# Kernel optimization log

Hardware: AMD Instinct MI355X
Metric: run time of the kernel (lower is better)

Reference implementation:

```python
import jax, jax.numpy as jnp
import numpy as np

B, S, E, H, L, D, G, V = 32, 256, 300, 256, 4000, 256, 512, 50000
LIN1, LIN2 = 512, 256  # linear_size


def _glorot(key, shape):
    fan_in, fan_out = shape[-1], shape[-2] if len(shape) > 1 else shape[-1]
    std = np.sqrt(2.0 / (fan_in + fan_out))
    return jax.random.normal(key, shape, dtype=jnp.float32) * std


def setup_inputs() -> dict:
    key = jax.random.key(0)
    ks = jax.random.split(key, 20)
    tokens = jax.random.randint(ks[0], (B, S), 1, V)  # avoid padding_idx=0
    emb_table = jax.random.normal(ks[1], (V, E), dtype=jnp.float32) * 0.1
    emb_table = emb_table.at[0].set(0.0)  # padding row
    # bidirectional LSTM (1 layer), torch gate order i,f,g,o
    w_ih_f = _glorot(ks[2], (4 * H, E));  w_hh_f = _glorot(ks[3], (4 * H, H))
    b_f = jnp.zeros((4 * H,), jnp.float32)
    w_ih_b = _glorot(ks[4], (4 * H, E));  w_hh_b = _glorot(ks[5], (4 * H, H))
    b_b = jnp.zeros((4 * H,), jnp.float32)
    # MLAttention: Linear(2H -> L, bias=False)
    attn_w = _glorot(ks[6], (L, 2 * H))
    # label graph branch
    label_emb = _glorot(ks[7], (L, D))
    adj_raw = (jax.random.uniform(ks[8], (L, L)) < 0.004).astype(jnp.float32)
    adj_raw = adj_raw + jnp.eye(L, dtype=jnp.float32)
    deg = jnp.sum(adj_raw, axis=1, keepdims=True)
    adj = adj_raw / deg  # row-normalized dense adjacency [L, L]
    gcn_w = _glorot(ks[9], (D, G));  gcn_b = jnp.zeros((G,), jnp.float32)
    # MLLinear([2H+G, 512, 256], 1)
    w1 = _glorot(ks[10], (2 * H + G, LIN1));  b1 = jnp.zeros((LIN1,), jnp.float32)
    w2 = _glorot(ks[11], (LIN1, LIN2));       b2 = jnp.zeros((LIN2,), jnp.float32)
    w_out = _glorot(ks[12], (LIN2, 1));       b_out = jnp.zeros((1,), jnp.float32)
    return dict(tokens=tokens, emb_table=emb_table,
                w_ih_f=w_ih_f, w_hh_f=w_hh_f, b_f=b_f,
                w_ih_b=w_ih_b, w_hh_b=w_hh_b, b_b=b_b,
                attn_w=attn_w, label_emb=label_emb, adj=adj,
                gcn_w=gcn_w, gcn_b=gcn_b,
                w1=w1, b1=b1, w2=w2, b2=b2, w_out=w_out, b_out=b_out)


def _lstm_dir(x_gates, w_hh, reverse):
    # x_gates: [B, S, 4H] precomputed input projections (+bias)
    def step(carry, xt):
        h, c = carry
        gates = xt + h @ w_hh.T
        i, f, g, o = jnp.split(gates, 4, axis=-1)
        c = jax.nn.sigmoid(f) * c + jax.nn.sigmoid(i) * jnp.tanh(g)
        h = jax.nn.sigmoid(o) * jnp.tanh(c)
        return (h, c), h
    b = x_gates.shape[0]
    init = (jnp.zeros((b, H), x_gates.dtype), jnp.zeros((b, H), x_gates.dtype))
    _, hs = jax.lax.scan(step, init, jnp.swapaxes(x_gates, 0, 1), reverse=reverse)
    return jnp.swapaxes(hs, 0, 1)  # [B, S, H]


def reference(tokens, emb_table, w_ih_f, w_hh_f, b_f, w_ih_b, w_hh_b, b_b,
              attn_w, label_emb, adj, gcn_w, gcn_b,
              w1, b1, w2, b2, w_out, b_out):
    masks = tokens != 0  # [B, S]
    emb_out = emb_table[tokens]  # [B, S, E]
    # bidirectional LSTM -> [B, S, 2H]
    gates_f = jnp.einsum('bse,ge->bsg', emb_out, w_ih_f) + b_f
    gates_b = jnp.einsum('bse,ge->bsg', emb_out, w_ih_b) + b_b
    rnn_out = jnp.concatenate([_lstm_dir(gates_f, w_hh_f, False),
                               _lstm_dir(gates_b, w_hh_b, True)], axis=-1)
    # MLAttention: per-label attention over sequence
    scores = jnp.einsum('bsh,lh->bls', rnn_out, attn_w)  # [B, L, S]
    scores = jnp.where(masks[:, None, :], scores, jnp.float32(-1e9))
    attn = jax.nn.softmax(scores, axis=-1)
    attn_out = jnp.einsum('bls,bsh->blh', attn, rnn_out)  # [B, L, 2H]
    # GCN over label graph: relu(A @ (X W) + b), single layer [D -> G]
    gcn_out = jax.nn.relu(adj @ (label_emb @ gcn_w) + gcn_b)  # [L, G]
    gcn_out = jnp.broadcast_to(gcn_out[None], (attn_out.shape[0], L, G))
    # concat fusion + MLLinear([2H+G, 512, 256], 1)
    x = jnp.concatenate([attn_out, gcn_out], axis=-1)  # [B, L, 2H+G]
    x = jax.nn.relu(x @ w1 + b1)
    x = jax.nn.relu(x @ w2 + b2)
    out = jnp.squeeze(x @ w_out + b_out, -1)  # [B, L]
    return out
```

## Files before the change

### kernel.cpp

```cpp
#include <hip/hip_runtime.h>
#include <hip/hip_bf16.h>
#include <math.h>


typedef __attribute__((ext_vector_type(8))) short bfrag;
typedef __attribute__((ext_vector_type(4))) float ffrag;

__device__ __forceinline__ ushort f2bf(float x) {
    union { float f; unsigned u; } c; c.f = x;
    const unsigned r = c.u + 0x7fffu + ((c.u >> 16) & 1u);
    return (ushort)(r >> 16);
}
__device__ __forceinline__ float bf2f(ushort h) {
    union { unsigned u; float f; } c; c.u = (unsigned)h << 16;
    return c.f;
}

template<bool BIAS, bool ADDROW, bool RELU, bool OUTF, bool OUTS>
__global__ __launch_bounds__(256) void mgemm_k(
    const ushort* __restrict__ A, const ushort* __restrict__ B,
    float* __restrict__ Cf, ushort* __restrict__ Cs,
    int M, int N, int K, int lda, int ldb, int ldc, int ldcs,
    long abs_, long bbs_, long cbs_, long csbs_,
    const float* __restrict__ bias,
    const float* __restrict__ addrow, int addmod, int ldadd)
{
    const int tid = threadIdx.x;
    const int ln = tid & 63;
    const int wv = tid >> 6;
    const int wm = wv >> 1, wn = wv & 1;
    const int m0 = blockIdx.x * 128, n0 = blockIdx.y * 128;
    const int z = blockIdx.z;
    A += (size_t)z * abs_;
    B += (size_t)z * bbs_;

    __shared__ ushort Ah[128 * 40], Al[128 * 40], Bh[128 * 40], Bl[128 * 40];

    ffrag acc[4][4];
#pragma unroll
    for (int i = 0; i < 4; ++i)
#pragma unroll
        for (int j = 0; j < 4; ++j) acc[i][j] = ffrag{0.f, 0.f, 0.f, 0.f};

    const int sr = tid >> 1;
    const int sk = (tid & 1) * 16;
    const int am = min(m0 + sr, M - 1);
    const int bn = n0 + sr;
    const int fr = ln & 15;
    const int fk = (ln >> 4) * 8;

    const ushort* arow = A + (size_t)am * lda + sk;
    const ushort* brow = B + (size_t)bn * ldb + sk;

    bfrag ah0, ah1, al0, al1, bh0, bh1, bl0, bl1;
    {
        const ushort* ap = arow;
        const ushort* bp = brow;
        ah0 = *(const bfrag*)ap;       ah1 = *(const bfrag*)(ap + 8);
        al0 = *(const bfrag*)(ap + K); al1 = *(const bfrag*)(ap + K + 8);
        bh0 = *(const bfrag*)bp;       bh1 = *(const bfrag*)(bp + 8);
        bl0 = *(const bfrag*)(bp + K); bl1 = *(const bfrag*)(bp + K + 8);
    }

    for (int k0 = 0; k0 < K; k0 += 32) {
        __syncthreads();
        *(bfrag*)&Ah[sr * 40 + sk] = ah0;  *(bfrag*)&Ah[sr * 40 + sk + 8] = ah1;
        *(bfrag*)&Al[sr * 40 + sk] = al0;  *(bfrag*)&Al[sr * 40 + sk + 8] = al1;
        *(bfrag*)&Bh[sr * 40 + sk] = bh0;  *(bfrag*)&Bh[sr * 40 + sk + 8] = bh1;
        *(bfrag*)&Bl[sr * 40 + sk] = bl0;  *(bfrag*)&Bl[sr * 40 + sk + 8] = bl1;
        __syncthreads();
        if (k0 + 32 < K) {
            const ushort* ap = arow + k0 + 32;
            const ushort* bp = brow + k0 + 32;
            ah0 = *(const bfrag*)ap;       ah1 = *(const bfrag*)(ap + 8);
            al0 = *(const bfrag*)(ap + K); al1 = *(const bfrag*)(ap + K + 8);
            bh0 = *(const bfrag*)bp;       bh1 = *(const bfrag*)(bp + 8);
            bl0 = *(const bfrag*)(bp + K); bl1 = *(const bfrag*)(bp + K + 8);
        }
        bfrag afh[4], afl[4];
#pragma unroll
        for (int i = 0; i < 4; ++i) {
            const int ar = (wm * 64 + i * 16 + fr) * 40 + fk;
            afh[i] = *(const bfrag*)&Ah[ar];
            afl[i] = *(const bfrag*)&Al[ar];
        }
#pragma unroll
        for (int j = 0; j < 4; ++j) {
            const int br = (wn * 64 + j * 16 + fr) * 40 + fk;
            const bfrag bfh = *(const bfrag*)&Bh[br];
            const bfrag bfl = *(const bfrag*)&Bl[br];
#pragma unroll
            for (int i = 0; i < 4; ++i) {
                acc[i][j] = __builtin_amdgcn_mfma_f32_16x16x32_bf16(afh[i], bfh, acc[i][j], 0, 0, 0);
                acc[i][j] = __builtin_amdgcn_mfma_f32_16x16x32_bf16(afh[i], bfl, acc[i][j], 0, 0, 0);
                acc[i][j] = __builtin_amdgcn_mfma_f32_16x16x32_bf16(afl[i], bfh, acc[i][j], 0, 0, 0);
            }
        }
    }

#pragma unroll
    for (int i = 0; i < 4; ++i) {
#pragma unroll
        for (int rg = 0; rg < 4; ++rg) {
            const int gm = m0 + wm * 64 + i * 16 + (ln >> 4) * 4 + rg;
            if (gm >= M) continue;
            const float* addp = ADDROW ? (addrow + (size_t)(gm % addmod) * ldadd) : nullptr;
#pragma unroll
            for (int j = 0; j < 4; ++j) {
                const int gn = n0 + wn * 64 + j * 16 + fr;
                float v = acc[i][j][rg];
                if (BIAS) v += bias[gn];
                if (ADDROW) v += addp[gn];
                if (RELU) v = fmaxf(v, 0.f);
                if (OUTF) Cf[(size_t)z * cbs_ + (size_t)gm * ldc + gn] = v;
                if (OUTS) {
                    const ushort h = f2bf(v);
                    const ushort l = f2bf(v - bf2f(h));
                    ushort* cp = Cs + (size_t)z * csbs_ + (size_t)gm * ldcs;
                    cp[gn] = h;
                    cp[N + gn] = l;
                }
            }
        }
    }
}

__global__ void gsplit_k(const float* __restrict__ src, const int* __restrict__ tok,
                         ushort* __restrict__ outp, int K, int Kpad)
{
    const int r = blockIdx.x;
    const float* s = src + (size_t)(tok ? tok[r] : r) * K;
    ushort* o = outp + (size_t)r * 2 * Kpad;
    for (int k = threadIdx.x; k < Kpad; k += blockDim.x) {
        const float x = (k < K) ? s[k] : 0.f;
        const ushort h = f2bf(x);
        const ushort l = f2bf(x - bf2f(h));
        o[k] = h;
        o[Kpad + k] = l;
    }
}

__global__ void split_k(const float* __restrict__ in, ushort* __restrict__ outp,
                        int rows, int K)
{
    const int i = blockIdx.x * 256 + threadIdx.x;
    if (i >= rows * K) return;
    const int r = i / K, k = i - r * K;
    const float x = in[i];
    const ushort h = f2bf(x);
    const ushort l = f2bf(x - bf2f(h));
    ushort* o = outp + (size_t)r * 2 * K;
    o[k] = h;
    o[K + k] = l;
}

__global__ __launch_bounds__(256) void tsplit_k(
    const float* __restrict__ in, ushort* __restrict__ outp,
    int R, int C, int ldin, long ibs, long obs)
{
    __shared__ float t[64][65];
    const int c0 = blockIdx.x * 64, r0 = blockIdx.y * 64;
    in   += (size_t)blockIdx.z * ibs;
    outp += (size_t)blockIdx.z * obs;
    const int tx = threadIdx.x & 15, ty = threadIdx.x >> 4;
#pragma unroll
    for (int i = 0; i < 4; ++i) {
        const int r = ty * 4 + i;
        const float4 v = *(const float4*)&in[(size_t)(r0 + r) * ldin + c0 + tx * 4];
        t[tx * 4 + 0][r] = v.x;
        t[tx * 4 + 1][r] = v.y;
        t[tx * 4 + 2][r] = v.z;
        t[tx * 4 + 3][r] = v.w;
    }
    __syncthreads();
    const int R2 = 2 * R;
#pragma unroll
    for (int i = 0; i < 4; ++i) {
        const int c = ty * 4 + i;
        ushort h[4], l[4];
#pragma unroll
        for (int k2 = 0; k2 < 4; ++k2) {
            const float x = t[c][tx * 4 + k2];
            h[k2] = f2bf(x);
            l[k2] = f2bf(x - bf2f(h[k2]));
        }
        uint2 hw, lw;
        hw.x = (unsigned)h[0] | ((unsigned)h[1] << 16);
        hw.y = (unsigned)h[2] | ((unsigned)h[3] << 16);
        lw.x = (unsigned)l[0] | ((unsigned)l[1] << 16);
        lw.y = (unsigned)l[2] | ((unsigned)l[3] << 16);
        *(uint2*)&outp[(size_t)(c0 + c) * R2 + r0 + tx * 4] = hw;
        *(uint2*)&outp[(size_t)(c0 + c) * R2 + R + r0 + tx * 4] = lw;
    }
}

__global__ __launch_bounds__(1024) void lstm_reg_k(
    const float* __restrict__ gxf, const float* __restrict__ gxb,
    const float* __restrict__ whf, const float* __restrict__ whb,
    float* __restrict__ rnn, float* hbuf, int* stamp)
{
    const int p = blockIdx.x;
    const int q = blockIdx.y;
    const int b = p >> 1, dir = p & 1;
    const float* xg = dir ? gxb : gxf;
    const float* W  = dir ? whb : whf;
    const int tid = threadIdx.x;
    const int wv = tid >> 6, lane = tid & 63;
    const int ul = lane >> 4;
    const int ks = (lane >> 2) & 3;
    const int gt = lane & 3;
    const int u  = wv * 4 + ul;
    const int grow = gt * 256 + q * 64 + u;

    float4 w[16];
    {
        const float4* wp = (const float4*)(W + (size_t)grow * 256 + ks * 64);
#pragma unroll
        for (int i = 0; i < 16; ++i) w[i] = wp[i];
    }

    __shared__ float h_lds[4 * 68];
    __shared__ float xg_lds[320];

    float* hb0 = hbuf + (size_t)p * 256;
    float* hb1 = hbuf + (size_t)(64 + p) * 256;
    int* sp = stamp + p * 16;

    const size_t xgb = (size_t)b * 256;
    const int g2 = (tid >> 6) * 256 + q * 64 + (tid & 63);
    float c = 0.f;
    float xg_cur = 0.f;
    if (tid < 256) xg_cur = xg[(xgb + (dir ? 255 : 0)) * 1024 + g2];

    for (int st = 0; st < 256; ++st) {
        const int ts = dir ? 255 - st : st;
        if (st > 0 && tid == 0) {
            while (true) {
                int s0 = __hip_atomic_load(&sp[0], __ATOMIC_RELAXED, __HIP_MEMORY_SCOPE_AGENT);
                int s1 = __hip_atomic_load(&sp[1], __ATOMIC_RELAXED, __HIP_MEMORY_SCOPE_AGENT);
                int s2 = __hip_atomic_load(&sp[2], __ATOMIC_RELAXED, __HIP_MEMORY_SCOPE_AGENT);
                int s3 = __hip_atomic_load(&sp[3], __ATOMIC_RELAXED, __HIP_MEMORY_SCOPE_AGENT);
                if (min(min(s0, s1), min(s2, s3)) >= st) break;
            }
        }
        __syncthreads();
        if (tid < 256) {
            float hv = 0.f;
            if (st > 0) {
                const float* src = (st & 1) ? hb0 : hb1;
                hv = __hip_atomic_load(&src[tid], __ATOMIC_RELAXED, __HIP_MEMORY_SCOPE_AGENT);
            }
            h_lds[(tid >> 6) * 68 + (tid & 63)] = hv;
            xg_lds[(tid & 63) * 5 + (tid >> 6)] = xg_cur;
        }
        __syncthreads();
        float acc = 0.f;
        {
            const float4* hp = (const float4*)&h_lds[ks * 68];
#pragma unroll
            for (int i = 0; i < 16; ++i) {
                const float4 hv = hp[i];
                acc = fmaf(w[i].x, hv.x, acc);
                acc = fmaf(w[i].y, hv.y, acc);
                acc = fmaf(w[i].z, hv.z, acc);
                acc = fmaf(w[i].w, hv.w, acc);
            }
        }
        acc += __shfl_xor(acc, 4);
        acc += __shfl_xor(acc, 8);
        const float g = acc + xg_lds[u * 5 + gt];
        const float t1 = __shfl_xor(g, 1);
        const float t2 = __shfl_xor(g, 2);
        const float t3 = __shfl_xor(t1, 2);
        const float g0 = (gt == 0) ? g : (gt == 1) ? t1 : (gt == 2) ? t2 : t3;
        const float g1 = (gt == 1) ? g : (gt == 0) ? t1 : (gt == 3) ? t2 : t3;
        const float g2v = (gt == 2) ? g : (gt == 3) ? t1 : (gt == 0) ? t2 : t3;
        const float g3v = (gt == 3) ? g : (gt == 2) ? t1 : (gt == 1) ? t2 : t3;
        const float si = 1.f / (1.f + __expf(-g0));
        const float sf = 1.f / (1.f + __expf(-g1));
        const float so = 1.f / (1.f + __expf(-g3v));
        const float tg = 1.f - 2.f / (__expf(2.f * g2v) + 1.f);
        c = sf * c + si * tg;
        const float tc = 1.f - 2.f / (__expf(2.f * c) + 1.f);
        const float hn = so * tc;
        if ((lane & 15) == 0) {
            float* dst = (st & 1) ? hb1 : hb0;
            __hip_atomic_store(&dst[q * 64 + u], hn, __ATOMIC_RELAXED, __HIP_MEMORY_SCOPE_AGENT);
            rnn[(xgb + ts) * 512 + (size_t)dir * 256 + q * 64 + u] = hn;
        }
        __syncthreads();
        if (tid == 0) {
            __hip_atomic_store(&sp[q], st + 1, __ATOMIC_RELAXED, __HIP_MEMORY_SCOPE_AGENT);
        }
        if (tid < 256 && st < 255) {
            const int tsn = dir ? 254 - st : st + 1;
            xg_cur = xg[(xgb + tsn) * 1024 + g2];
        }
    }
}

__global__ void init_cnt_k(int* stamp) {
    const int i = blockIdx.x * blockDim.x + threadIdx.x;
    if (i < 1024) stamp[i] = 0;
}

__global__ __launch_bounds__(256) void softmax_split_k(
    float* __restrict__ sc, const int* __restrict__ tokens, int b0)
{
    const int bb = blockIdx.y;
    const int l  = blockIdx.x * 4 + (threadIdx.x >> 6);
    const int lane = threadIdx.x & 63;
    float* row = sc + ((size_t)bb * 4000 + l) * 256;
    const int* tk = tokens + (size_t)(b0 + bb) * 256;
    float4 v = *(const float4*)&row[lane * 4];
    const int4 tv = *(const int4*)&tk[lane * 4];
    if (tv.x == 0) v.x = -1e9f;
    if (tv.y == 0) v.y = -1e9f;
    if (tv.z == 0) v.z = -1e9f;
    if (tv.w == 0) v.w = -1e9f;
    float mx = fmaxf(fmaxf(v.x, v.y), fmaxf(v.z, v.w));
    for (int o = 32; o > 0; o >>= 1) mx = fmaxf(mx, __shfl_xor(mx, o));
    v.x = __expf(v.x - mx); v.y = __expf(v.y - mx);
    v.z = __expf(v.z - mx); v.w = __expf(v.w - mx);
    float s = v.x + v.y + v.z + v.w;
    for (int o = 32; o > 0; o >>= 1) s += __shfl_xor(s, o);
    const float inv = 1.f / s;
    const float p0 = v.x * inv, p1 = v.y * inv, p2 = v.z * inv, p3 = v.w * inv;
    const ushort h0 = f2bf(p0), h1 = f2bf(p1), h2 = f2bf(p2), h3 = f2bf(p3);
    const ushort l0 = f2bf(p0 - bf2f(h0)), l1 = f2bf(p1 - bf2f(h1));
    const ushort l2 = f2bf(p2 - bf2f(h2)), l3 = f2bf(p3 - bf2f(h3));
    ushort* orow = (ushort*)row;
    uint2 hw, lw;
    hw.x = (unsigned)h0 | ((unsigned)h1 << 16);
    hw.y = (unsigned)h2 | ((unsigned)h3 << 16);
    lw.x = (unsigned)l0 | ((unsigned)l1 << 16);
    lw.y = (unsigned)l2 | ((unsigned)l3 << 16);
    *(uint2*)&orow[lane * 4] = hw;
    *(uint2*)&orow[256 + lane * 4] = lw;
}

__global__ __launch_bounds__(256) void spmm_k(
    const float* __restrict__ adj, const float* __restrict__ tmp,
    const float* __restrict__ bias, float* __restrict__ outp)
{
    const int l = blockIdx.x;
    __shared__ int   idxs[4][256];
    __shared__ float vals[4][256];
    __shared__ int   cnts[4];
    const int t = threadIdx.x;
    const int w = t >> 6, lane = t & 63;
    const float* arow = adj + (size_t)l * 4000;
    int cnt = 0;
    for (int r = 0; r < 16; ++r) {
        const int o = r * 64 + lane;
        const int j = w * 1000 + o;
        const float a = (o < 1000) ? arow[j] : 0.f;
        const unsigned long long mk = __ballot(a != 0.f);
        if (a != 0.f) {
            const int pos = cnt + __popcll(mk & ((1ull << lane) - 1ull));
            if (pos < 256) { idxs[w][pos] = j; vals[w][pos] = a; }
        }
        cnt += __popcll(mk);
    }
    if (lane == 0) cnts[w] = min(cnt, 256);
    __syncthreads();
    const int c0 = t * 2;
    float a0 = 0.f, a1 = 0.f;
    for (int ww = 0; ww < 4; ++ww) {
        const int n = cnts[ww];
        for (int e = 0; e < n; ++e) {
            const float a = vals[ww][e];
            const float2 tv = *(const float2*)&tmp[(size_t)idxs[ww][e] * 512 + c0];
            a0 = fmaf(a, tv.x, a0);
            a1 = fmaf(a, tv.y, a1);
        }
    }
    float2 res;
    res.x = fmaxf(a0 + bias[c0], 0.f);
    res.y = fmaxf(a1 + bias[c0 + 1], 0.f);
    *(float2*)&outp[(size_t)l * 512 + c0] = res;
}

__global__ __launch_bounds__(256) void out_k(
    const float* __restrict__ x2, const float* __restrict__ w_out,
    const float* __restrict__ b_out, float* __restrict__ outp, int b0)
{
    const int r = blockIdx.x * 4 + (threadIdx.x >> 6);
    const int lane = threadIdx.x & 63;
    const float4 xv = *(const float4*)&x2[(size_t)r * 256 + lane * 4];
    const float4 wv = *(const float4*)&w_out[lane * 4];
    float s = xv.x * wv.x + xv.y * wv.y + xv.z * wv.z + xv.w * wv.w;
    for (int o = 32; o > 0; o >>= 1) s += __shfl_xor(s, o);
    if (lane == 0) {
        const int bb = r / 4000, l = r - bb * 4000;
        outp[(size_t)(b0 + bb) * 4000 + l] = s + b_out[0];
    }
}

extern "C" void kernel_launch(void* const* d_in, const int* in_sizes, int n_in,
                              void* d_out, int out_size, void* d_ws, size_t ws_size,
                              hipStream_t stream)
{
    const int*   tokens    = (const int*)  d_in[0];
    const float* emb       = (const float*)d_in[1];
    const float* w_ih_f    = (const float*)d_in[2];
    const float* w_hh_f    = (const float*)d_in[3];
    const float* b_f       = (const float*)d_in[4];
    const float* w_ih_b    = (const float*)d_in[5];
    const float* w_hh_b    = (const float*)d_in[6];
    const float* b_b       = (const float*)d_in[7];
    const float* attn_w    = (const float*)d_in[8];
    const float* label_emb = (const float*)d_in[9];
    const float* adj       = (const float*)d_in[10];
    const float* gcn_w     = (const float*)d_in[11];
    const float* gcn_b     = (const float*)d_in[12];
    const float* w1        = (const float*)d_in[13];
    const float* b1        = (const float*)d_in[14];
    const float* w2        = (const float*)d_in[15];
    const float* b2        = (const float*)d_in[16];
    const float* w_out     = (const float*)d_in[17];
    const float* b_out     = (const float*)d_in[18];
    float* outp = (float*)d_out;
    float* wsf  = (float*)d_ws;

    const size_t off_gf  = 0;
    const size_t off_gb  = 8388608;
    const size_t off_rnn = 16777216;
    const size_t off_tmp = 20971520;
    const size_t off_go  = 23019520;
    const size_t off_ctr = 25067520;
    const size_t base_end = 27115520;
    const size_t S_sz = 10829824;
    const size_t have = ws_size / 4;
    int NB = 1; size_t offS = off_gf, offC = off_gf + S_sz;
    {
        const int tiers[6] = {32, 16, 8, 4, 2, 0};
        bool found = false;
        for (int t = 0; tiers[t]; ++t) {
            if (have >= base_end + S_sz + (size_t)tiers[t] * 5120000) {
                NB = tiers[t]; offS = base_end; offC = base_end + S_sz; found = true; break;
            }
        }
        if (!found && have >= base_end + S_sz) { NB = 2; offS = base_end; offC = off_gf; }
    }

    float* gates_f = wsf + off_gf;
    float* gates_b = wsf + off_gb;
    float* rnn     = wsf + off_rnn;
    float* gcn_tmp = wsf + off_tmp;
    float* gcn_out = wsf + off_go;
    float* contrib = wsf + off_ctr;
    float* hbuf    = wsf + off_tmp;
    int*   stamp   = (int*)(wsf + off_tmp + 32768);

    const size_t off_esp = (offS == off_gf) ? off_rnn : offS;
    ushort* esplit  = (ushort*)(wsf + off_esp);
    ushort* wsplitf = esplit + (size_t)8192 * 640;
    ushort* wsplitb = wsplitf + (size_t)1024 * 640;

    ushort* attn_ws16 = (ushort*)(wsf + offS);
    ushort* w1t16     = (ushort*)(wsf + offS + 2048000);
    ushort* w2t16     = (ushort*)(wsf + offS + 2310144);
    ushort* rnn_nt16  = (ushort*)(wsf + offS + 2441216);
    ushort* rnnT16    = (ushort*)(wsf + offS + 6635520);

    float*  scoresb = wsf + offC;
    ushort* attn16  = (ushort*)(wsf + offC + (size_t)NB * 1024000);
    ushort* x116    = (ushort*)(wsf + offC + (size_t)NB * 1024000 + (size_t)NB * 2048000);
    float*  x2b     = scoresb;

    ushort* le16   = (ushort*)(wsf + offC);
    ushort* gw16   = le16 + (size_t)4000 * 512;
    ushort* go16   = gw16 + (size_t)512 * 512;
    ushort* w1b16  = go16 + (size_t)4000 * 1024;

    init_cnt_k<<<4, 256, 0, stream>>>(stamp);

    gsplit_k<<<8192, 256, 0, stream>>>(emb, tokens, esplit, 300, 320);
    gsplit_k<<<1024, 256, 0, stream>>>(w_ih_f, nullptr, wsplitf, 300, 320);
    gsplit_k<<<1024, 256, 0, stream>>>(w_ih_b, nullptr, wsplitb, 300, 320);
    mgemm_k<true, false, false, true, false><<<dim3(64, 8, 1), 256, 0, stream>>>(
        esplit, wsplitf, gates_f, nullptr,
        8192, 1024, 320, 640, 640, 1024, 0,
        0L, 0L, 0L, 0L, b_f, nullptr, 1, 0);
    mgemm_k<true, false, false, true, false><<<dim3(64, 8, 1), 256, 0, stream>>>(
        esplit, wsplitb, gates_b, nullptr,
        8192, 1024, 320, 640, 640, 1024, 0,
        0L, 0L, 0L, 0L, b_b, nullptr, 1, 0);

    lstm_reg_k<<<dim3(64, 4), 1024, 0, stream>>>(
        gates_f, gates_b, w_hh_f, w_hh_b, rnn, hbuf, stamp);

    split_k<<<16384, 256, 0, stream>>>(rnn, rnn_nt16, 8192, 512);
    tsplit_k<<<dim3(8, 4, 32), 256, 0, stream>>>(rnn, rnnT16, 256, 512, 512, 131072, 262144);
    split_k<<<8000, 256, 0, stream>>>(attn_w, attn_ws16, 4000, 512);
    tsplit_k<<<dim3(8, 8, 1), 256, 0, stream>>>(w1, w1t16, 512, 512, 512, 0, 0);
    tsplit_k<<<dim3(4, 8, 1), 256, 0, stream>>>(w2, w2t16, 512, 256, 256, 0, 0);

    split_k<<<4000, 256, 0, stream>>>(label_emb, le16, 4000, 256);
    tsplit_k<<<dim3(8, 4, 1), 256, 0, stream>>>(gcn_w, gw16, 256, 512, 512, 0, 0);
    mgemm_k<false, false, false, true, false><<<dim3(32, 4, 1), 256, 0, stream>>>(
        le16, gw16, gcn_tmp, nullptr,
        4000, 512, 256, 512, 512, 512, 0,
        0L, 0L, 0L, 0L, nullptr, nullptr, 1, 0);
    spmm_k<<<dim3(4000), 256, 0, stream>>>(adj, gcn_tmp, gcn_b, gcn_out);
    split_k<<<8000, 256, 0, stream>>>(gcn_out, go16, 4000, 512);
    tsplit_k<<<dim3(8, 8, 1), 256, 0, stream>>>(w1 + (size_t)512 * 512, w1b16, 512, 512, 512, 0, 0);
    mgemm_k<true, false, false, true, false><<<dim3(32, 4, 1), 256, 0, stream>>>(
        go16, w1b16, contrib, nullptr,
        4000, 512, 512, 1024, 1024, 512, 0,
        0L, 0L, 0L, 0L, b1, nullptr, 1, 0);

    for (int b0 = 0; b0 < 32; b0 += NB) {
        const int nb = (32 - b0 < NB) ? (32 - b0) : NB;
        mgemm_k<false, false, false, true, false><<<dim3(32, 2, nb), 256, 0, stream>>>(
            attn_ws16, rnn_nt16 + (size_t)b0 * 262144, scoresb, nullptr,
            4000, 256, 512, 1024, 1024, 256, 0,
            0L, 262144L, 1024000L, 0L, nullptr, nullptr, 1, 0);
        softmax_split_k<<<dim3(1000, nb), 256, 0, stream>>>(scoresb, tokens, b0);
        mgemm_k<false, false, false, false, true><<<dim3(32, 4, nb), 256, 0, stream>>>(
            (const ushort*)scoresb, rnnT16 + (size_t)b0 * 262144, nullptr, attn16,
            4000, 512, 256, 512, 512, 0, 1024,
            2048000L, 262144L, 0L, 4096000L, nullptr, nullptr, 1, 0);
        mgemm_k<false, true, true, false, true><<<dim3((nb * 4000 + 127) / 128, 4, 1), 256, 0, stream>>>(
            attn16, w1t16, nullptr, x116,
            nb * 4000, 512, 512, 1024, 1024, 0, 1024,
            0L, 0L, 0L, 0L, nullptr, contrib, 4000, 512);
        mgemm_k<true, false, true, true, false><<<dim3((nb * 4000 + 127) / 128, 2, 1), 256, 0, stream>>>(
            x116, w2t16, x2b, nullptr,
            nb * 4000, 256, 512, 1024, 1024, 256, 0,
            0L, 0L, 0L, 0L, b2, nullptr, 1, 0);
        out_k<<<dim3(nb * 1000), 256, 0, stream>>>(x2b, w_out, b_out, outp, b0);
    }
}
```

Measured before the change: 1.770 ms.

## Fuse final output dot product into second MLP GEMM epilogue and swap grid axes

Adds an OUTDOT epilogue to the GEMM that applies bias, ReLU and the w_out dot product in registers, reduces across lanes and warps, and writes per-N-block partial sums. A small outsum kernel then adds the two partials and b_out. This removes the write and re-read of the full x2 activation buffer and the separate out_k launch. All GEMM launches also swap grid x/y so that N tiles vary fastest, which can change L2 reuse of the A tiles.

```diff
diff --git a/kernel.cpp b/kernel.cpp
--- a/kernel.cpp
+++ b/kernel.cpp
@@ -16,20 +16,22 @@
     return c.f;
 }
 
-template<bool BIAS, bool ADDROW, bool RELU, bool OUTF, bool OUTS>
+template<bool BIAS, bool ADDROW, bool RELU, bool OUTF, bool OUTS, bool OUTDOT>
 __global__ __launch_bounds__(256) void mgemm_k(
     const ushort* __restrict__ A, const ushort* __restrict__ B,
     float* __restrict__ Cf, ushort* __restrict__ Cs,
     int M, int N, int K, int lda, int ldb, int ldc, int ldcs,
     long abs_, long bbs_, long cbs_, long csbs_,
     const float* __restrict__ bias,
-    const float* __restrict__ addrow, int addmod, int ldadd)
+    const float* __restrict__ addrow, int addmod, int ldadd,
+    const float* __restrict__ dotw, float* __restrict__ pd)
 {
     const int tid = threadIdx.x;
     const int ln = tid & 63;
     const int wv = tid >> 6;
     const int wm = wv >> 1, wn = wv & 1;
-    const int m0 = blockIdx.x * 128, n0 = blockIdx.y * 128;
+    const int n0 = blockIdx.x * 128;
+    const int m0 = blockIdx.y * 128;
     const int z = blockIdx.z;
     A += (size_t)z * abs_;
     B += (size_t)z * bbs_;
@@ -96,6 +98,62 @@
                 acc[i][j] = __builtin_amdgcn_mfma_f32_16x16x32_bf16(afl[i], bfh, acc[i][j], 0, 0, 0);
             }
         }
+    }
+
+    if (OUTDOT) {
+        float wv4[4], bv4[4];
+#pragma unroll
+        for (int j = 0; j < 4; ++j) {
+            const int gn = n0 + wn * 64 + j * 16 + fr;
+            wv4[j] = dotw[gn];
+            bv4[j] = BIAS ? bias[gn] : 0.f;
+        }
+        float rsum[16];
+#pragma unroll
+        for (int i = 0; i < 4; ++i) {
+#pragma unroll
+            for (int rg = 0; rg < 4; ++rg) {
+                const int gm = m0 + wm * 64 + i * 16 + (ln >> 4) * 4 + rg;
+                float p = 0.f;
+                if (gm < M) {
+#pragma unroll
+                    for (int j = 0; j < 4; ++j) {
+                        float v = acc[i][j][rg] + bv4[j];
+                        if (RELU) v = fmaxf(v, 0.f);
+                        p = fmaf(v, wv4[j], p);
+                    }
+                }
+                rsum[i * 4 + rg] = p;
+            }
+        }
+#pragma unroll
+        for (int t = 0; t < 16; ++t) {
+            rsum[t] += __shfl_xor(rsum[t], 1);
+            rsum[t] += __shfl_xor(rsum[t], 2);
+            rsum[t] += __shfl_xor(rsum[t], 4);
+            rsum[t] += __shfl_xor(rsum[t], 8);
+        }
+        float* pdls = (float*)Ah;
+        __syncthreads();
+        if (wn == 0 && fr == 0) {
+#pragma unroll
+            for (int i = 0; i < 4; ++i)
+#pragma unroll
+                for (int rg = 0; rg < 4; ++rg)
+                    pdls[wm * 64 + i * 16 + (ln >> 4) * 4 + rg] = rsum[i * 4 + rg];
+        }
+        __syncthreads();
+        if (wn == 1 && fr == 0) {
+#pragma unroll
+            for (int i = 0; i < 4; ++i)
+#pragma unroll
+                for (int rg = 0; rg < 4; ++rg) {
+                    const int lr = wm * 64 + i * 16 + (ln >> 4) * 4 + rg;
+                    const int gm = m0 + lr;
+                    if (gm < M) pd[(size_t)blockIdx.x * M + gm] = pdls[lr] + rsum[i * 4 + rg];
+                }
+        }
+        return;
     }
 
 #pragma unroll
@@ -123,6 +181,15 @@
             }
         }
     }
+}
+
+__global__ void outsum_k(const float* __restrict__ pd, const float* __restrict__ b_out,
+                         float* __restrict__ outp, int M, int b0)
+{
+    const int r = blockIdx.x * 256 + threadIdx.x;
+    if (r >= M) return;
+    const int bb = r / 4000, l = r - bb * 4000;
+    outp[(size_t)(b0 + bb) * 4000 + l] = (pd[r] + pd[(size_t)M + r]) + b_out[0];
 }
 
 __global__ void gsplit_k(const float* __restrict__ src, const int* __restrict__ tok,
@@ -381,22 +448,6 @@
     *(float2*)&outp[(size_t)l * 512 + c0] = res;
 }
 
-__global__ __launch_bounds__(256) void out_k(
-    const float* __restrict__ x2, const float* __restrict__ w_out,
-    const float* __restrict__ b_out, float* __restrict__ outp, int b0)
-{
-    const int r = blockIdx.x * 4 + (threadIdx.x >> 6);
-    const int lane = threadIdx.x & 63;
-    const float4 xv = *(const float4*)&x2[(size_t)r * 256 + lane * 4];
-    const float4 wv = *(const float4*)&w_out[lane * 4];
-    float s = xv.x * wv.x + xv.y * wv.y + xv.z * wv.z + xv.w * wv.w;
-    for (int o = 32; o > 0; o >>= 1) s += __shfl_xor(s, o);
-    if (lane == 0) {
-        const int bb = r / 4000, l = r - bb * 4000;
-        outp[(size_t)(b0 + bb) * 4000 + l] = s + b_out[0];
-    }
-}
-
 extern "C" void kernel_launch(void* const* d_in, const int* in_sizes, int n_in,
                               void* d_out, int out_size, void* d_ws, size_t ws_size,
                               hipStream_t stream)
@@ -467,7 +518,7 @@
     float*  scoresb = wsf + offC;
     ushort* attn16  = (ushort*)(wsf + offC + (size_t)NB * 1024000);
     ushort* x116    = (ushort*)(wsf + offC + (size_t)NB * 1024000 + (size_t)NB * 2048000);
-    float*  x2b     = scoresb;
+    float*  pd      = scoresb;
 
     ushort* le16   = (ushort*)(wsf + offC);
     ushort* gw16   = le16 + (size_t)4000 * 512;
@@ -479,14 +530,14 @@
     gsplit_k<<<8192, 256, 0, stream>>>(emb, tokens, esplit, 300, 320);
     gsplit_k<<<1024, 256, 0, stream>>>(w_ih_f, nullptr, wsplitf, 300, 320);
     gsplit_k<<<1024, 256, 0, stream>>>(w_ih_b, nullptr, wsplitb, 300, 320);
-    mgemm_k<true, false, false, true, false><<<dim3(64, 8, 1), 256, 0, stream>>>(
+    mgemm_k<true, false, false, true, false, false><<<dim3(8, 64, 1), 256, 0, stream>>>(
         esplit, wsplitf, gates_f, nullptr,
         8192, 1024, 320, 640, 640, 1024, 0,
-        0L, 0L, 0L, 0L, b_f, nullptr, 1, 0);
-    mgemm_k<true, false, false, true, false><<<dim3(64, 8, 1), 256, 0, stream>>>(
+        0L, 0L, 0L, 0L, b_f, nullptr, 1, 0, nullptr, nullptr);
+    mgemm_k<true, false, false, true, false, false><<<dim3(8, 64, 1), 256, 0, stream>>>(
         esplit, wsplitb, gates_b, nullptr,
         8192, 1024, 320, 640, 640, 1024, 0,
-        0L, 0L, 0L, 0L, b_b, nullptr, 1, 0);
+        0L, 0L, 0L, 0L, b_b, nullptr, 1, 0, nullptr, nullptr);
 
     lstm_reg_k<<<dim3(64, 4), 1024, 0, stream>>>(
         gates_f, gates_b, w_hh_f, w_hh_b, rnn, hbuf, stamp);
@@ -499,37 +550,37 @@
 
     split_k<<<4000, 256, 0, stream>>>(label_emb, le16, 4000, 256);
     tsplit_k<<<dim3(8, 4, 1), 256, 0, stream>>>(gcn_w, gw16, 256, 512, 512, 0, 0);
-    mgemm_k<false, false, false, true, false><<<dim3(32, 4, 1), 256, 0, stream>>>(
+    mgemm_k<false, false, false, true, false, false><<<dim3(4, 32, 1), 256, 0, stream>>>(
         le16, gw16, gcn_tmp, nullptr,
         4000, 512, 256, 512, 512, 512, 0,
-        0L, 0L, 0L, 0L, nullptr, nullptr, 1, 0);
+        0L, 0L, 0L, 0L, nullptr, nullptr, 1, 0, nullptr, nullptr);
     spmm_k<<<dim3(4000), 256, 0, stream>>>(adj, gcn_tmp, gcn_b, gcn_out);
     split_k<<<8000, 256, 0, stream>>>(gcn_out, go16, 4000, 512);
     tsplit_k<<<dim3(8, 8, 1), 256, 0, stream>>>(w1 + (size_t)512 * 512, w1b16, 512, 512, 512, 0, 0);
-    mgemm_k<true, false, false, true, false><<<dim3(32, 4, 1), 256, 0, stream>>>(
+    mgemm_k<true, false, false, true, false, false><<<dim3(4, 32, 1), 256, 0, stream>>>(
         go16, w1b16, contrib, nullptr,
         4000, 512, 512, 1024, 1024, 512, 0,
-        0L, 0L, 0L, 0L, b1, nullptr, 1, 0);
+        0L, 0L, 0L, 0L, b1, nullptr, 1, 0, nullptr, nullptr);
 
     for (int b0 = 0; b0 < 32; b0 += NB) {
         const int nb = (32 - b0 < NB) ? (32 - b0) : NB;
-        mgemm_k<false, false, false, true, false><<<dim3(32, 2, nb), 256, 0, stream>>>(
+        mgemm_k<false, false, false, true, false, false><<<dim3(2, 32, nb), 256, 0, stream>>>(
             attn_ws16, rnn_nt16 + (size_t)b0 * 262144, scoresb, nullptr,
             4000, 256, 512, 1024, 1024, 256, 0,
-            0L, 262144L, 1024000L, 0L, nullptr, nullptr, 1, 0);
+            0L, 262144L, 1024000L, 0L, nullptr, nullptr, 1, 0, nullptr, nullptr);
         softmax_split_k<<<dim3(1000, nb), 256, 0, stream>>>(scoresb, tokens, b0);
-        mgemm_k<false, false, false, false, true><<<dim3(32, 4, nb), 256, 0, stream>>>(
+        mgemm_k<false, false, false, false, true, false><<<dim3(4, 32, nb), 256, 0, stream>>>(
             (const ushort*)scoresb, rnnT16 + (size_t)b0 * 262144, nullptr, attn16,
             4000, 512, 256, 512, 512, 0, 1024,
-            2048000L, 262144L, 0L, 4096000L, nullptr, nullptr, 1, 0);
-        mgemm_k<false, true, true, false, true><<<dim3((nb * 4000 + 127) / 128, 4, 1), 256, 0, stream>>>(
+            2048000L, 262144L, 0L, 4096000L, nullptr, nullptr, 1, 0, nullptr, nullptr);
+        mgemm_k<false, true, true, false, true, false><<<dim3(4, (nb * 4000 + 127) / 128, 1), 256, 0, stream>>>(
             attn16, w1t16, nullptr, x116,
             nb * 4000, 512, 512, 1024, 1024, 0, 1024,
-            0L, 0L, 0L, 0L, nullptr, contrib, 4000, 512);
-        mgemm_k<true, false, true, true, false><<<dim3((nb * 4000 + 127) / 128, 2, 1), 256, 0, stream>>>(
-            x116, w2t16, x2b, nullptr,
-            nb * 4000, 256, 512, 1024, 1024, 256, 0,
-            0L, 0L, 0L, 0L, b2, nullptr, 1, 0);
-        out_k<<<dim3(nb * 1000), 256, 0, stream>>>(x2b, w_out, b_out, outp, b0);
-    }
-}
+            0L, 0L, 0L, 0L, nullptr, contrib, 4000, 512, nullptr, nullptr);
+        mgemm_k<true, false, true, false, false, true><<<dim3(2, (nb * 4000 + 127) / 128, 1), 256, 0, stream>>>(
+            x116, w2t16, nullptr, nullptr,
+            nb * 4000, 256, 512, 1024, 1024, 0, 0,
+            0L, 0L, 0L, 0L, b2, nullptr, 1, 0, w_out, pd);
+        outsum_k<<<(nb * 4000 + 255) / 256, 256, 0, stream>>>(pd, b_out, outp, nb * 4000, b0);
+    }
+}
```

After: 1.757 ms (median of 2 runs). Within noise of the previous version (-0.7%).
